# Performance work log

Hardware: AMD Instinct MI355X
Metric: run time of the kernel (lower is better)

The kernel has to match this reference:

```python
import jax, jax.numpy as jnp
import numpy as np

N = 50000       # nodes
E = 1_600_000   # edges (avg degree 32)
NFEAT = 256
NHID = 128
NCLASS = 128    # must equal NHID for the gated skip connection to type-check


def setup_inputs() -> dict:
    key = jax.random.key(0)
    ks = jax.random.split(key, 16)
    g = 0.02  # xavier gain used in the module
    inp = {
        "x": jax.random.normal(ks[0], (N, NFEAT), dtype=jnp.float32),
        "row": jax.random.randint(ks[1], (E,), 0, N, dtype=jnp.int32),
        "col": jax.random.randint(ks[2], (E,), 0, N, dtype=jnp.int32),
        # GatedSkipConnection params (shared across the three skip calls)
        "W_sc": jax.random.normal(ks[3], (NFEAT, NHID), dtype=jnp.float32) * 0.05,
        "W_ci": jax.random.normal(ks[4], (NHID, NHID), dtype=jnp.float32) * 0.05,
        "b_ci": jnp.zeros((NHID,), dtype=jnp.float32),
        "W_co": jax.random.normal(ks[5], (NHID, NHID), dtype=jnp.float32) * 0.05,
        "b_co": jnp.zeros((NHID,), dtype=jnp.float32),
        # GraphSAGE layer weights: [2*in, out], bias [1, out] (init to 0 per module)
        "W0": jax.random.normal(ks[6], (2 * NFEAT, NHID), dtype=jnp.float32) * g,
        "b0": jnp.zeros((1, NHID), dtype=jnp.float32),
        "W1": jax.random.normal(ks[7], (2 * NHID, NHID), dtype=jnp.float32) * g,
        "b1": jnp.zeros((1, NHID), dtype=jnp.float32),
        "W2": jax.random.normal(ks[8], (2 * NHID, NCLASS), dtype=jnp.float32) * g,
        "b2": jnp.zeros((1, NCLASS), dtype=jnp.float32),
        # fc0: Linear(nhid, nclass)
        "Wf": jax.random.normal(ks[9], (NHID, NCLASS), dtype=jnp.float32) * 0.05,
        "bf": jnp.zeros((NCLASS,), dtype=jnp.float32),
    }
    return inp


def _sage(x, row, col, inv_deg, W, b):
    # adj @ x : sum source features x[col] into destination rows `row`
    agg = jax.ops.segment_sum(x[col], row, num_segments=N)  # [N, d]
    agg = agg * inv_deg[:, None]                            # degree normalization
    support = jnp.concatenate([x, agg], axis=1)             # [N, 2d]
    return support @ W + b


def _gsc(in_x, out_x, W_sc, W_ci, b_ci, W_co, b_co):
    in_x = in_x @ W_sc if in_x.shape[1] != out_x.shape[1] else in_x
    z = jax.nn.sigmoid(in_x @ W_ci + b_ci + out_x @ W_co + b_co)
    return z * out_x + (1.0 - z) * in_x


def reference(x, row, col, W_sc, W_ci, b_ci, W_co, b_co,
              W0, b0, W1, b1, W2, b2, Wf, bf):
    deg = jax.ops.segment_sum(jnp.ones((E,), x.dtype), row, num_segments=N)
    inv_deg = 1.0 / jnp.maximum(deg, 1.0)  # guard isolated nodes

    residual = x
    o1 = _sage(x, row, col, inv_deg, W0, b0)
    o3 = jax.nn.relu(_gsc(residual, o1, W_sc, W_ci, b_ci, W_co, b_co))
    o4 = _sage(o3, row, col, inv_deg, W1, b1)
    o6 = jax.nn.relu(_gsc(residual, o4, W_sc, W_ci, b_ci, W_co, b_co))
    o7 = _sage(o6, row, col, inv_deg, W2, b2)
    o8 = _gsc(residual, o7, W_sc, W_ci, b_ci, W_co, b_co)
    return o8 @ Wf + bf
```

## Files before the change

### kernel.cpp

```cpp
#include <hip/hip_runtime.h>
#include <hip/hip_bf16.h>
#include <hip/hip_fp16.h>
#include <math.h>

#define NN 50000
#define EE 1600000
#define NFEAT 256
#define NHID 128
#define RNG 12500
#define NPASS 4
#define CPAD 16

typedef _Float16 f16;
typedef _Float16 f16x8 __attribute__((ext_vector_type(8)));
typedef _Float16 f16x4 __attribute__((ext_vector_type(4)));
typedef float f32x4 __attribute__((ext_vector_type(4)));

struct WPtrs {
    const float* s[10];
    f16* d[10];
};

__global__ __launch_bounds__(256) void k_prep(const float* __restrict__ x,
                                              f16* __restrict__ xh, int n4,
                                              int* __restrict__ cnt, int nz4,
                                              WPtrs wp, int wtotal,
                                              int zb0, int wb0, int wblocks) {
    int b = blockIdx.x;
    if (b < zb0) {
        int i = b * 256 + threadIdx.x;
        if (i < n4) {
            float4 v = reinterpret_cast<const float4*>(x)[i];
            f16x4 h = {(f16)v.x, (f16)v.y, (f16)v.z, (f16)v.w};
            reinterpret_cast<f16x4*>(xh)[i] = h;
        }
    } else if (b < wb0) {
        int i = (b - zb0) * 256 + threadIdx.x;
        if (i < nz4) reinterpret_cast<int4*>(cnt)[i] = make_int4(0, 0, 0, 0);
    } else {
        for (int idx = (b - wb0) * 256 + threadIdx.x; idx < wtotal;
             idx += wblocks * 256) {
            int wsel, rem, K;
            if (idx < 3 * 32768) { wsel = idx >> 15; rem = idx & 32767; K = 256; }
            else { int t = idx - 3 * 32768; wsel = 3 + (t >> 14); rem = t & 16383; K = 128; }
            int k = rem >> 7, c = rem & 127;
            wp.d[wsel][c * K + k] = (f16)wp.s[wsel][rem];
        }
    }
}

__global__ void k_slot(const int* __restrict__ row, int* __restrict__ cnt,
                       int* __restrict__ epack, int e) {
    int i = blockIdx.x * 256 + threadIdx.x;
    if (i < e) {
        int r = row[i];
        int s = atomicAdd(&cnt[(size_t)r * CPAD], 1);
        epack[i] = (s << 16) | r;
    }
}

__global__ void k_scan1(const int* __restrict__ cnt, int* __restrict__ bsum, int n) {
    __shared__ int s[256];
    int t = threadIdx.x;
    int i = blockIdx.x * 256 + t;
    s[t] = (i < n) ? cnt[(size_t)i * CPAD] : 0;
    __syncthreads();
    for (int off = 128; off > 0; off >>= 1) {
        if (t < off) s[t] += s[t + off];
        __syncthreads();
    }
    if (t == 0) bsum[blockIdx.x] = s[0];
}

__global__ void k_scan3(const int* __restrict__ cnt, const int* __restrict__ bsum,
                        int* __restrict__ rp, float* __restrict__ invd,
                        int n, int nb) {
    __shared__ int buf[2][256];
    __shared__ int bpre[2][256];
    int t = threadIdx.x;

    bpre[0][t] = (t < nb) ? bsum[t] : 0;
    __syncthreads();
    int bs = 0;
    for (int off = 1; off < 256; off <<= 1) {
        int v = bpre[bs][t];
        if (t >= off) v += bpre[bs][t - off];
        bpre[bs ^ 1][t] = v;
        bs ^= 1;
        __syncthreads();
    }
    int base = (blockIdx.x == 0) ? 0 : bpre[bs][blockIdx.x - 1];

    int i = blockIdx.x * 256 + t;
    int v = (i < n) ? cnt[(size_t)i * CPAD] : 0;
    buf[0][t] = v;
    __syncthreads();
    int sel = 0;
    for (int off = 1; off < 256; off <<= 1) {
        int x = buf[sel][t];
        if (t >= off) x += buf[sel][t - off];
        buf[sel ^ 1][t] = x;
        sel ^= 1;
        __syncthreads();
    }
    int incl = buf[sel][t];
    int excl = incl - v;
    if (i < n) {
        rp[i] = base + excl;
        invd[i] = 1.0f / fmaxf((float)v, 1.0f);
        if (i == n - 1) rp[n] = base + incl;
    }
}

__global__ void k_fill(const int* __restrict__ epack, const int* __restrict__ col,
                       const int* __restrict__ rp, int* __restrict__ ci, int e) {
    int i = blockIdx.x * 256 + threadIdx.x;
    if (i >= e) return;
    int pk = epack[i];
    int r = pk & 0xFFFF;
    int lo = blockIdx.y * RNG;
    if (r >= lo && r < lo + RNG) ci[rp[r] + (pk >> 16)] = col[i];
}

__global__ __launch_bounds__(256) void k_agg2h(const f16* __restrict__ P,
                                               const int* __restrict__ rp,
                                               const int* __restrict__ ci,
                                               const float* __restrict__ invd,
                                               const f16* __restrict__ T,
                                               f16* __restrict__ OUT, int n) {
    int node = blockIdx.x * 16 + (threadIdx.x >> 4);
    if (node >= n) return;
    int lane = threadIdx.x & 15;
    int s = rp[node], e = rp[node + 1];
    float acc[8];
#pragma unroll
    for (int q = 0; q < 8; ++q) acc[q] = 0.0f;
    int j = s;
    for (; j + 8 <= e; j += 8) {
        f16x8 v[8];
#pragma unroll
        for (int u = 0; u < 8; ++u)
            v[u] = *reinterpret_cast<const f16x8*>(P + (size_t)ci[j + u] * 128 + lane * 8);
#pragma unroll
        for (int q = 0; q < 8; ++q)
            acc[q] += (((float)v[0][q] + (float)v[1][q]) + ((float)v[2][q] + (float)v[3][q])) +
                      (((float)v[4][q] + (float)v[5][q]) + ((float)v[6][q] + (float)v[7][q]));
    }
    for (; j < e; ++j) {
        f16x8 v0 = *reinterpret_cast<const f16x8*>(P + (size_t)ci[j] * 128 + lane * 8);
#pragma unroll
        for (int q = 0; q < 8; ++q) acc[q] += (float)v0[q];
    }
    float scl = invd[node];
    f16x8 tv = *reinterpret_cast<const f16x8*>(T + (size_t)node * 128 + lane * 8);
    f16x8 o;
#pragma unroll
    for (int q = 0; q < 8; ++q) o[q] = (f16)((float)tv[q] + scl * acc[q]);
    *reinterpret_cast<f16x8*>(OUT + (size_t)node * 128 + lane * 8) = o;
}

#define LDSSTR 40

__device__ __forceinline__ void stage_A(const f16* __restrict__ A, f16* sA,
                                        int row0, int K, int kb, int tid, int n) {
    int r = tid >> 2, ch = tid & 3;
    int gr = row0 + r;
    uint4 v = make_uint4(0, 0, 0, 0);
    if (gr < n) v = *reinterpret_cast<const uint4*>(A + (size_t)gr * K + kb + ch * 8);
    *reinterpret_cast<uint4*>(sA + r * LDSSTR + ch * 8) = v;
}

__device__ __forceinline__ void stage_B(const f16* __restrict__ Wt, f16* sB,
                                        int K, int kb, int tid) {
#pragma unroll
    for (int i = 0; i < 2; ++i) {
        int idx = tid + i * 256;
        int c = idx >> 2, ch = idx & 3;
        uint4 v = *reinterpret_cast<const uint4*>(Wt + (size_t)c * K + kb + ch * 8);
        *reinterpret_cast<uint4*>(sB + c * LDSSTR + ch * 8) = v;
    }
}

template <int K, int NW, bool F32OUT>
__global__ __launch_bounds__(256) void k_mgemm(const f16* __restrict__ A,
                                               const f16* __restrict__ Wt0,
                                               const f16* __restrict__ Wt1,
                                               const f16* __restrict__ Wt2,
                                               const float* __restrict__ bias0,
                                               void* __restrict__ C0,
                                               void* __restrict__ C1,
                                               void* __restrict__ C2, int n) {
    __shared__ f16 sA[64 * LDSSTR];
    __shared__ f16 sB[128 * LDSSTR];

    const f16* Wt = Wt0;
    const float* bias = bias0;
    void* C = C0;
    if (NW > 1 && blockIdx.y == 1) { Wt = Wt1; bias = nullptr; C = C1; }
    if (NW > 2 && blockIdx.y == 2) { Wt = Wt2; bias = nullptr; C = C2; }

    const int tid = threadIdx.x;
    const int row0 = blockIdx.x * 64;
    const int wid = tid >> 6, l = tid & 63;
    const int wr = wid >> 1, wc = wid & 1;
    const int lr = l & 15, lk = (l >> 4) * 8;

    f32x4 acc[2][4];
#pragma unroll
    for (int m = 0; m < 2; ++m)
#pragma unroll
        for (int q = 0; q < 4; ++q) acc[m][q] = (f32x4){0.f, 0.f, 0.f, 0.f};

    for (int kt = 0; kt < K / 32; ++kt) {
        stage_A(A, sA, row0, K, kt * 32, tid, n);
        stage_B(Wt, sB, K, kt * 32, tid);
        __syncthreads();
        f16x8 aF[2], bF[4];
#pragma unroll
        for (int m = 0; m < 2; ++m)
            aF[m] = *reinterpret_cast<f16x8*>(sA + (wr * 32 + m * 16 + lr) * LDSSTR + lk);
#pragma unroll
        for (int q = 0; q < 4; ++q)
            bF[q] = *reinterpret_cast<f16x8*>(sB + (wc * 64 + q * 16 + lr) * LDSSTR + lk);
#pragma unroll
        for (int m = 0; m < 2; ++m)
#pragma unroll
            for (int q = 0; q < 4; ++q)
                acc[m][q] = __builtin_amdgcn_mfma_f32_16x16x32_f16(aF[m], bF[q],
                                                                   acc[m][q], 0, 0, 0);
        __syncthreads();
    }

    const int lr4 = (l >> 4) * 4;
#pragma unroll
    for (int m = 0; m < 2; ++m)
#pragma unroll
        for (int q = 0; q < 4; ++q) {
            int c = wc * 64 + q * 16 + (l & 15);
            float b = bias ? bias[c] : 0.0f;
#pragma unroll
            for (int reg = 0; reg < 4; ++reg) {
                int r = row0 + wr * 32 + m * 16 + lr4 + reg;
                if (r >= n) continue;
                float v = acc[m][q][reg] + b;
                if (F32OUT) ((float*)C)[(size_t)r * 128 + c] = v;
                else        ((f16*)C)[(size_t)r * 128 + c] = (f16)v;
            }
        }
}

#define FSTR 136

template <int RELU, bool CLS>
__global__ __launch_bounds__(256) void k_fused(const f16* __restrict__ Asc,
                                               const f16* __restrict__ At0,
                                               const f16* __restrict__ Wci,
                                               const f16* __restrict__ Wco,
                                               const f16* __restrict__ WtT,
                                               const f16* __restrict__ WtP,
                                               const float* __restrict__ bci,
                                               const float* __restrict__ bco,
                                               const float* __restrict__ bias2,
                                               f16* __restrict__ To,
                                               f16* __restrict__ Po,
                                               float* __restrict__ Fo, int n) {
    __shared__ f16 lsc[64 * FSTR];
    __shared__ f16 lt0[64 * FSTR];
    __shared__ f16 lt1[64 * FSTR];

    const int tid = threadIdx.x;
    const int row0 = blockIdx.x * 64;
    const int wid = tid >> 6, l = tid & 63;
    const int wr = wid >> 1, wc = wid & 1;
    const int lr = l & 15, lk = (l >> 4) * 8;
    const int lr4 = (l >> 4) * 4;

#pragma unroll
    for (int i = 0; i < 4; ++i) {
        int idx = tid + i * 256;
        int r = idx >> 4, ch = idx & 15;
        int gr = row0 + r;
        uint4 vs = make_uint4(0, 0, 0, 0), vt = make_uint4(0, 0, 0, 0);
        if (gr < n) {
            vs = *reinterpret_cast<const uint4*>(Asc + (size_t)gr * 128 + ch * 8);
            vt = *reinterpret_cast<const uint4*>(At0 + (size_t)gr * 128 + ch * 8);
        }
        *reinterpret_cast<uint4*>(lsc + r * FSTR + ch * 8) = vs;
        *reinterpret_cast<uint4*>(lt0 + r * FSTR + ch * 8) = vt;
    }
    __syncthreads();

    f32x4 accG[2][4];
#pragma unroll
    for (int m = 0; m < 2; ++m)
#pragma unroll
        for (int q = 0; q < 4; ++q) accG[m][q] = (f32x4){0.f, 0.f, 0.f, 0.f};

#pragma unroll
    for (int kt = 0; kt < 4; ++kt) {
        f16x8 aS[2], aT[2], bC[4], bO[4];
#pragma unroll
        for (int m = 0; m < 2; ++m) {
            int rr = (wr * 32 + m * 16 + lr) * FSTR + kt * 32 + lk;
            aS[m] = *reinterpret_cast<const f16x8*>(lsc + rr);
            aT[m] = *reinterpret_cast<const f16x8*>(lt0 + rr);
        }
#pragma unroll
        for (int q = 0; q < 4; ++q) {
            int c = wc * 64 + q * 16 + lr;
            bC[q] = *reinterpret_cast<const f16x8*>(Wci + (size_t)c * 128 + kt * 32 + lk);
            bO[q] = *reinterpret_cast<const f16x8*>(Wco + (size_t)c * 128 + kt * 32 + lk);
        }
#pragma unroll
        for (int m = 0; m < 2; ++m)
#pragma unroll
            for (int q = 0; q < 4; ++q) {
                accG[m][q] = __builtin_amdgcn_mfma_f32_16x16x32_f16(aS[m], bC[q],
                                                                    accG[m][q], 0, 0, 0);
                accG[m][q] = __builtin_amdgcn_mfma_f32_16x16x32_f16(aT[m], bO[q],
                                                                    accG[m][q], 0, 0, 0);
            }
    }

#pragma unroll
    for (int m = 0; m < 2; ++m)
#pragma unroll
        for (int q = 0; q < 4; ++q) {
            int c = wc * 64 + q * 16 + (l & 15);
            float bb = bci[c] + bco[c];
#pragma unroll
            for (int reg = 0; reg < 4; ++reg) {
                int lrow = wr * 32 + m * 16 + lr4 + reg;
                float v = accG[m][q][reg] + bb;
                float z = 1.0f / (1.0f + __expf(-v));
                float o = (float)lt0[lrow * FSTR + c];
                float s = (float)lsc[lrow * FSTR + c];
                float t1v = z * o + (1.0f - z) * s;
                if (RELU) t1v = fmaxf(t1v, 0.0f);
                lt1[lrow * FSTR + c] = (f16)t1v;
            }
        }
    __syncthreads();

    f32x4 accT[2][4], accP[2][4];
#pragma unroll
    for (int m = 0; m < 2; ++m)
#pragma unroll
        for (int q = 0; q < 4; ++q) {
            accT[m][q] = (f32x4){0.f, 0.f, 0.f, 0.f};
            accP[m][q] = (f32x4){0.f, 0.f, 0.f, 0.f};
        }

#pragma unroll
    for (int kt = 0; kt < 4; ++kt) {
        f16x8 aF[2], bT[4], bP[4];
#pragma unroll
        for (int m = 0; m < 2; ++m)
            aF[m] = *reinterpret_cast<const f16x8*>(
                lt1 + (wr * 32 + m * 16 + lr) * FSTR + kt * 32 + lk);
#pragma unroll
        for (int q = 0; q < 4; ++q) {
            int c = wc * 64 + q * 16 + lr;
            bT[q] = *reinterpret_cast<const f16x8*>(WtT + (size_t)c * 128 + kt * 32 + lk);
            if (!CLS)
                bP[q] = *reinterpret_cast<const f16x8*>(WtP + (size_t)c * 128 + kt * 32 + lk);
        }
#pragma unroll
        for (int m = 0; m < 2; ++m)
#pragma unroll
            for (int q = 0; q < 4; ++q) {
                accT[m][q] = __builtin_amdgcn_mfma_f32_16x16x32_f16(aF[m], bT[q],
                                                                    accT[m][q], 0, 0, 0);
                if (!CLS)
                    accP[m][q] = __builtin_amdgcn_mfma_f32_16x16x32_f16(aF[m], bP[q],
                                                                        accP[m][q], 0, 0, 0);
            }
    }

#pragma unroll
    for (int m = 0; m < 2; ++m)
#pragma unroll
        for (int q = 0; q < 4; ++q) {
            int c = wc * 64 + q * 16 + (l & 15);
            float b = bias2[c];
#pragma unroll
            for (int reg = 0; reg < 4; ++reg) {
                int r = row0 + wr * 32 + m * 16 + lr4 + reg;
                if (r >= n) continue;
                if (CLS) {
                    Fo[(size_t)r * 128 + c] = accT[m][q][reg] + b;
                } else {
                    To[(size_t)r * 128 + c] = (f16)(accT[m][q][reg] + b);
                    Po[(size_t)r * 128 + c] = (f16)accP[m][q][reg];
                }
            }
        }
}

extern "C" void kernel_launch(void* const* d_in, const int* in_sizes, int n_in,
                              void* d_out, int out_size, void* d_ws, size_t ws_size,
                              hipStream_t stream) {
    const float* x    = (const float*)d_in[0];
    const int*   row  = (const int*)d_in[1];
    const int*   col  = (const int*)d_in[2];
    const float* W_sc = (const float*)d_in[3];
    const float* W_ci = (const float*)d_in[4];
    const float* b_ci = (const float*)d_in[5];
    const float* W_co = (const float*)d_in[6];
    const float* b_co = (const float*)d_in[7];
    const float* W0   = (const float*)d_in[8];
    const float* b0   = (const float*)d_in[9];
    const float* W1   = (const float*)d_in[10];
    const float* b1   = (const float*)d_in[11];
    const float* W2   = (const float*)d_in[12];
    const float* b2   = (const float*)d_in[13];
    const float* Wf   = (const float*)d_in[14];
    const float* bf   = (const float*)d_in[15];
    float* out = (float*)d_out;

    char* p = (char*)d_ws;
    auto alloc = [&](size_t bytes) {
        char* q = p;
        p += (bytes + 255) & ~(size_t)255;
        return q;
    };
    int*   cnt   = (int*)alloc((size_t)NN * CPAD * 4);
    int*   rp    = (int*)alloc((NN + 1) * 4);
    int*   bsum  = (int*)alloc(256 * 4);
    float* invd  = (float*)alloc(NN * 4);
    int*   ci    = (int*)alloc(EE * 4);
    int*   epack = (int*)alloc(EE * 4);
    f16*   x_h   = (f16*)alloc((size_t)NN * 256 * 2);
    f16*   sc_h  = (f16*)alloc((size_t)NN * 128 * 2);
    f16*   T_h   = (f16*)alloc((size_t)NN * 128 * 2);
    f16*   P_h   = (f16*)alloc((size_t)NN * 128 * 2);
    f16*   t0_h  = (f16*)alloc((size_t)NN * 128 * 2);
    f16* W0t_t = (f16*)alloc(256 * 128 * 2);
    f16* W0b_t = (f16*)alloc(256 * 128 * 2);
    f16* Wsc_t = (f16*)alloc(256 * 128 * 2);
    f16* W1t_t = (f16*)alloc(128 * 128 * 2);
    f16* W1b_t = (f16*)alloc(128 * 128 * 2);
    f16* W2t_t = (f16*)alloc(128 * 128 * 2);
    f16* W2b_t = (f16*)alloc(128 * 128 * 2);
    f16* Wci_t = (f16*)alloc(128 * 128 * 2);
    f16* Wco_t = (f16*)alloc(128 * 128 * 2);
    f16* Wf_t  = (f16*)alloc(128 * 128 * 2);

    const int NB_N  = (NN + 255) / 256;
    const int NB_E  = (EE + 255) / 256;
    const int GB    = (NN + 63) / 64;
    const int AGG_B = (NN + 15) / 16;

    const int N4   = NN * 256 / 4;
    const int NZ4  = NN * CPAD / 4;
    const int ZB0  = (N4 + 255) / 256;
    const int WB0  = ZB0 + (NZ4 + 255) / 256;
    const int WBLK = 84;
    const int WTOT = 3 * 32768 + 7 * 16384;
    WPtrs wp;
    wp.s[0] = W0;             wp.d[0] = W0t_t;
    wp.s[1] = W0 + 256 * 128; wp.d[1] = W0b_t;
    wp.s[2] = W_sc;           wp.d[2] = Wsc_t;
    wp.s[3] = W1;             wp.d[3] = W1t_t;
    wp.s[4] = W1 + 128 * 128; wp.d[4] = W1b_t;
    wp.s[5] = W2;             wp.d[5] = W2t_t;
    wp.s[6] = W2 + 128 * 128; wp.d[6] = W2b_t;
    wp.s[7] = W_ci;           wp.d[7] = Wci_t;
    wp.s[8] = W_co;           wp.d[8] = Wco_t;
    wp.s[9] = Wf;             wp.d[9] = Wf_t;
    k_prep<<<WB0 + WBLK, 256, 0, stream>>>(x, x_h, N4, cnt, NZ4, wp, WTOT,
                                           ZB0, WB0, WBLK);

    k_slot<<<NB_E, 256, 0, stream>>>(row, cnt, epack, EE);
    k_scan1<<<NB_N, 256, 0, stream>>>(cnt, bsum, NN);
    k_scan3<<<NB_N, 256, 0, stream>>>(cnt, bsum, rp, invd, NN, NB_N);
    k_fill<<<dim3(NB_E, NPASS), 256, 0, stream>>>(epack, col, rp, ci, EE);

    k_mgemm<256, 3, false><<<dim3(GB, 3), 256, 0, stream>>>(
        x_h, W0t_t, W0b_t, Wsc_t, b0, T_h, P_h, sc_h, NN);
    k_agg2h<<<AGG_B, 256, 0, stream>>>(P_h, rp, ci, invd, T_h, t0_h, NN);

    k_fused<1, false><<<GB, 256, 0, stream>>>(
        sc_h, t0_h, Wci_t, Wco_t, W1t_t, W1b_t, b_ci, b_co, b1,
        T_h, P_h, nullptr, NN);
    k_agg2h<<<AGG_B, 256, 0, stream>>>(P_h, rp, ci, invd, T_h, t0_h, NN);

    k_fused<1, false><<<GB, 256, 0, stream>>>(
        sc_h, t0_h, Wci_t, Wco_t, W2t_t, W2b_t, b_ci, b_co, b2,
        T_h, P_h, nullptr, NN);
    k_agg2h<<<AGG_B, 256, 0, stream>>>(P_h, rp, ci, invd, T_h, t0_h, NN);

    k_fused<0, true><<<GB, 256, 0, stream>>>(
        sc_h, t0_h, Wci_t, Wco_t, Wf_t, nullptr, b_ci, b_co, bf,
        nullptr, nullptr, out, NN);
}
```

Before: 544.7 us.

## Fuse edge slotting with first GEMM and shuffle-broadcast neighbor indices in aggregation

Merges the atomic edge-slot kernel and the first three-way GEMM into one launch, interleaving GEMM blocks among slot blocks so the memory-bound atomics overlap with MFMA work and one launch is removed. The aggregation kernel now loads 16 neighbor indices cooperatively per 16-lane group and broadcasts them with shuffles, issuing 16 gathers in flight instead of 8 with per-lane redundant index loads. The tail handles the remainder with clamped indices and predicated accumulation. This raises register pressure in the aggregation kernel and makes the fused kernel's register and LDS footprint apply to the slot blocks as well.

```diff
diff --git a/kernel.cpp b/kernel.cpp
--- a/kernel.cpp
+++ b/kernel.cpp
@@ -10,6 +10,9 @@
 #define RNG 12500
 #define NPASS 4
 #define CPAD 16
+#define GB 782
+#define NGEMM (GB * 3)
+#define NB_E 6250
 
 typedef _Float16 f16;
 typedef _Float16 f16x8 __attribute__((ext_vector_type(8)));
@@ -49,13 +52,118 @@
     }
 }
 
-__global__ void k_slot(const int* __restrict__ row, int* __restrict__ cnt,
-                       int* __restrict__ epack, int e) {
-    int i = blockIdx.x * 256 + threadIdx.x;
-    if (i < e) {
-        int r = row[i];
-        int s = atomicAdd(&cnt[(size_t)r * CPAD], 1);
-        epack[i] = (s << 16) | r;
+#define LDSSTR 40
+
+__device__ __forceinline__ void stage_A(const f16* __restrict__ A, f16* sA,
+                                        int row0, int K, int kb, int tid, int n) {
+    int r = tid >> 2, ch = tid & 3;
+    int gr = row0 + r;
+    uint4 v = make_uint4(0, 0, 0, 0);
+    if (gr < n) v = *reinterpret_cast<const uint4*>(A + (size_t)gr * K + kb + ch * 8);
+    *reinterpret_cast<uint4*>(sA + r * LDSSTR + ch * 8) = v;
+}
+
+__device__ __forceinline__ void stage_B(const f16* __restrict__ Wt, f16* sB,
+                                        int K, int kb, int tid) {
+#pragma unroll
+    for (int i = 0; i < 2; ++i) {
+        int idx = tid + i * 256;
+        int c = idx >> 2, ch = idx & 3;
+        uint4 v = *reinterpret_cast<const uint4*>(Wt + (size_t)c * K + kb + ch * 8);
+        *reinterpret_cast<uint4*>(sB + c * LDSSTR + ch * 8) = v;
+    }
+}
+
+__device__ void gemm0_body(int bx, int by, f16* sA, f16* sB,
+                           const f16* __restrict__ A,
+                           const f16* __restrict__ Wt0,
+                           const f16* __restrict__ Wt1,
+                           const f16* __restrict__ Wt2,
+                           const float* __restrict__ bias0,
+                           f16* __restrict__ C0, f16* __restrict__ C1,
+                           f16* __restrict__ C2, int n) {
+    constexpr int K = 256;
+    const f16* Wt = Wt0;
+    const float* bias = bias0;
+    f16* C = C0;
+    if (by == 1) { Wt = Wt1; bias = nullptr; C = C1; }
+    if (by == 2) { Wt = Wt2; bias = nullptr; C = C2; }
+
+    const int tid = threadIdx.x;
+    const int row0 = bx * 64;
+    const int wid = tid >> 6, l = tid & 63;
+    const int wr = wid >> 1, wc = wid & 1;
+    const int lr = l & 15, lk = (l >> 4) * 8;
+
+    f32x4 acc[2][4];
+#pragma unroll
+    for (int m = 0; m < 2; ++m)
+#pragma unroll
+        for (int q = 0; q < 4; ++q) acc[m][q] = (f32x4){0.f, 0.f, 0.f, 0.f};
+
+    for (int kt = 0; kt < K / 32; ++kt) {
+        stage_A(A, sA, row0, K, kt * 32, tid, n);
+        stage_B(Wt, sB, K, kt * 32, tid);
+        __syncthreads();
+        f16x8 aF[2], bF[4];
+#pragma unroll
+        for (int m = 0; m < 2; ++m)
+            aF[m] = *reinterpret_cast<f16x8*>(sA + (wr * 32 + m * 16 + lr) * LDSSTR + lk);
+#pragma unroll
+        for (int q = 0; q < 4; ++q)
+            bF[q] = *reinterpret_cast<f16x8*>(sB + (wc * 64 + q * 16 + lr) * LDSSTR + lk);
+#pragma unroll
+        for (int m = 0; m < 2; ++m)
+#pragma unroll
+            for (int q = 0; q < 4; ++q)
+                acc[m][q] = __builtin_amdgcn_mfma_f32_16x16x32_f16(aF[m], bF[q],
+                                                                   acc[m][q], 0, 0, 0);
+        __syncthreads();
+    }
+
+    const int lr4 = (l >> 4) * 4;
+#pragma unroll
+    for (int m = 0; m < 2; ++m)
+#pragma unroll
+        for (int q = 0; q < 4; ++q) {
+            int c = wc * 64 + q * 16 + (l & 15);
+            float b = bias ? bias[c] : 0.0f;
+#pragma unroll
+            for (int reg = 0; reg < 4; ++reg) {
+                int r = row0 + wr * 32 + m * 16 + lr4 + reg;
+                if (r >= n) continue;
+                C[(size_t)r * 128 + c] = (f16)(acc[m][q][reg] + b);
+            }
+        }
+}
+
+__global__ __launch_bounds__(256) void k_slotgemm(
+    const int* __restrict__ row, int* __restrict__ cnt,
+    int* __restrict__ epack, int e,
+    const f16* __restrict__ A,
+    const f16* __restrict__ Wt0, const f16* __restrict__ Wt1,
+    const f16* __restrict__ Wt2, const float* __restrict__ bias0,
+    f16* __restrict__ C0, f16* __restrict__ C1, f16* __restrict__ C2, int n) {
+    __shared__ f16 sA[64 * LDSSTR];
+    __shared__ f16 sB[128 * LDSSTR];
+
+    int p = blockIdx.x / 11, k = blockIdx.x % 11;
+    bool isG = (k == 2) || (k == 6) || (k == 9);
+    if (isG) {
+        int idx = (k == 2) ? 0 : ((k == 6) ? 1 : 2);
+        int g = p * 3 + idx;
+        if (g >= NGEMM) return;
+        gemm0_body(g % GB, g / GB, sA, sB, A, Wt0, Wt1, Wt2, bias0, C0, C1, C2, n);
+    } else {
+        int rank = k - (k > 2) - (k > 6) - (k > 9);
+        int s = p * 8 + rank;
+        if (s >= NB_E) return;
+        int i = s * 256 + threadIdx.x;
+        if (i < e) {
+            int r = row[i];
+            int sl = atomicAdd(&cnt[(size_t)r * CPAD], 1);
+            epack[i] = (sl << 16) | r;
+        }
     }
 }
 
@@ -135,118 +243,43 @@
     float acc[8];
 #pragma unroll
     for (int q = 0; q < 8; ++q) acc[q] = 0.0f;
+
     int j = s;
-    for (; j + 8 <= e; j += 8) {
-        f16x8 v[8];
-#pragma unroll
-        for (int u = 0; u < 8; ++u)
-            v[u] = *reinterpret_cast<const f16x8*>(P + (size_t)ci[j + u] * 128 + lane * 8);
-#pragma unroll
-        for (int q = 0; q < 8; ++q)
-            acc[q] += (((float)v[0][q] + (float)v[1][q]) + ((float)v[2][q] + (float)v[3][q])) +
-                      (((float)v[4][q] + (float)v[5][q]) + ((float)v[6][q] + (float)v[7][q]));
-    }
-    for (; j < e; ++j) {
-        f16x8 v0 = *reinterpret_cast<const f16x8*>(P + (size_t)ci[j] * 128 + lane * 8);
-#pragma unroll
-        for (int q = 0; q < 8; ++q) acc[q] += (float)v0[q];
-    }
+    for (; j + 16 <= e; j += 16) {
+        int civ = ci[j + lane];
+        f16x8 v[16];
+#pragma unroll
+        for (int u = 0; u < 16; ++u) {
+            int nb = __shfl(civ, u, 16);
+            v[u] = *reinterpret_cast<const f16x8*>(P + (size_t)nb * 128 + lane * 8);
+        }
+#pragma unroll
+        for (int u = 0; u < 16; ++u)
+#pragma unroll
+            for (int q = 0; q < 8; ++q) acc[q] += (float)v[u][q];
+    }
+    int rem = e - j;
+    if (rem > 0) {
+        int civ = ci[j + (lane < rem ? lane : rem - 1)];
+        f16x8 v[16];
+#pragma unroll
+        for (int u = 0; u < 16; ++u) {
+            int nb = __shfl(civ, u, 16);
+            v[u] = *reinterpret_cast<const f16x8*>(P + (size_t)nb * 128 + lane * 8);
+        }
+#pragma unroll
+        for (int u = 0; u < 16; ++u)
+            if (u < rem)
+#pragma unroll
+                for (int q = 0; q < 8; ++q) acc[q] += (float)v[u][q];
+    }
+
     float scl = invd[node];
     f16x8 tv = *reinterpret_cast<const f16x8*>(T + (size_t)node * 128 + lane * 8);
     f16x8 o;
 #pragma unroll
     for (int q = 0; q < 8; ++q) o[q] = (f16)((float)tv[q] + scl * acc[q]);
     *reinterpret_cast<f16x8*>(OUT + (size_t)node * 128 + lane * 8) = o;
-}
-
-#define LDSSTR 40
-
-__device__ __forceinline__ void stage_A(const f16* __restrict__ A, f16* sA,
-                                        int row0, int K, int kb, int tid, int n) {
-    int r = tid >> 2, ch = tid & 3;
-    int gr = row0 + r;
-    uint4 v = make_uint4(0, 0, 0, 0);
-    if (gr < n) v = *reinterpret_cast<const uint4*>(A + (size_t)gr * K + kb + ch * 8);
-    *reinterpret_cast<uint4*>(sA + r * LDSSTR + ch * 8) = v;
-}
-
-__device__ __forceinline__ void stage_B(const f16* __restrict__ Wt, f16* sB,
-                                        int K, int kb, int tid) {
-#pragma unroll
-    for (int i = 0; i < 2; ++i) {
-        int idx = tid + i * 256;
-        int c = idx >> 2, ch = idx & 3;
-        uint4 v = *reinterpret_cast<const uint4*>(Wt + (size_t)c * K + kb + ch * 8);
-        *reinterpret_cast<uint4*>(sB + c * LDSSTR + ch * 8) = v;
-    }
-}
-
-template <int K, int NW, bool F32OUT>
-__global__ __launch_bounds__(256) void k_mgemm(const f16* __restrict__ A,
-                                               const f16* __restrict__ Wt0,
-                                               const f16* __restrict__ Wt1,
-                                               const f16* __restrict__ Wt2,
-                                               const float* __restrict__ bias0,
-                                               void* __restrict__ C0,
-                                               void* __restrict__ C1,
-                                               void* __restrict__ C2, int n) {
-    __shared__ f16 sA[64 * LDSSTR];
-    __shared__ f16 sB[128 * LDSSTR];
-
-    const f16* Wt = Wt0;
-    const float* bias = bias0;
-    void* C = C0;
-    if (NW > 1 && blockIdx.y == 1) { Wt = Wt1; bias = nullptr; C = C1; }
-    if (NW > 2 && blockIdx.y == 2) { Wt = Wt2; bias = nullptr; C = C2; }
-
-    const int tid = threadIdx.x;
-    const int row0 = blockIdx.x * 64;
-    const int wid = tid >> 6, l = tid & 63;
-    const int wr = wid >> 1, wc = wid & 1;
-    const int lr = l & 15, lk = (l >> 4) * 8;
-
-    f32x4 acc[2][4];
-#pragma unroll
-    for (int m = 0; m < 2; ++m)
-#pragma unroll
-        for (int q = 0; q < 4; ++q) acc[m][q] = (f32x4){0.f, 0.f, 0.f, 0.f};
-
-    for (int kt = 0; kt < K / 32; ++kt) {
-        stage_A(A, sA, row0, K, kt * 32, tid, n);
-        stage_B(Wt, sB, K, kt * 32, tid);
-        __syncthreads();
-        f16x8 aF[2], bF[4];
-#pragma unroll
-        for (int m = 0; m < 2; ++m)
-            aF[m] = *reinterpret_cast<f16x8*>(sA + (wr * 32 + m * 16 + lr) * LDSSTR + lk);
-#pragma unroll
-        for (int q = 0; q < 4; ++q)
-            bF[q] = *reinterpret_cast<f16x8*>(sB + (wc * 64 + q * 16 + lr) * LDSSTR + lk);
-#pragma unroll
-        for (int m = 0; m < 2; ++m)
-#pragma unroll
-            for (int q = 0; q < 4; ++q)
-                acc[m][q] = __builtin_amdgcn_mfma_f32_16x16x32_f16(aF[m], bF[q],
-                                                                   acc[m][q], 0, 0, 0);
-        __syncthreads();
-    }
-
-    const int lr4 = (l >> 4) * 4;
-#pragma unroll
-    for (int m = 0; m < 2; ++m)
-#pragma unroll
-        for (int q = 0; q < 4; ++q) {
-            int c = wc * 64 + q * 16 + (l & 15);
-            float b = bias ? bias[c] : 0.0f;
-#pragma unroll
-            for (int reg = 0; reg < 4; ++reg) {
-                int r = row0 + wr * 32 + m * 16 + lr4 + reg;
-                if (r >= n) continue;
-                float v = acc[m][q][reg] + b;
-                if (F32OUT) ((float*)C)[(size_t)r * 128 + c] = v;
-                else        ((f16*)C)[(size_t)r * 128 + c] = (f16)v;
-            }
-        }
 }
 
 #define FSTR 136
@@ -447,9 +480,8 @@
     f16* Wf_t  = (f16*)alloc(128 * 128 * 2);
 
     const int NB_N  = (NN + 255) / 256;
-    const int NB_E  = (EE + 255) / 256;
-    const int GB    = (NN + 63) / 64;
     const int AGG_B = (NN + 15) / 16;
+    const int MGRID = GB * 11;
 
     const int N4   = NN * 256 / 4;
     const int NZ4  = NN * CPAD / 4;
@@ -471,13 +503,14 @@
     k_prep<<<WB0 + WBLK, 256, 0, stream>>>(x, x_h, N4, cnt, NZ4, wp, WTOT,
                                            ZB0, WB0, WBLK);
 
-    k_slot<<<NB_E, 256, 0, stream>>>(row, cnt, epack, EE);
+    k_slotgemm<<<MGRID, 256, 0, stream>>>(row, cnt, epack, EE,
+                                          x_h, W0t_t, W0b_t, Wsc_t, b0,
+                                          T_h, P_h, sc_h, NN);
+
     k_scan1<<<NB_N, 256, 0, stream>>>(cnt, bsum, NN);
     k_scan3<<<NB_N, 256, 0, stream>>>(cnt, bsum, rp, invd, NN, NB_N);
     k_fill<<<dim3(NB_E, NPASS), 256, 0, stream>>>(epack, col, rp, ci, EE);
 
-    k_mgemm<256, 3, false><<<dim3(GB, 3), 256, 0, stream>>>(
-        x_h, W0t_t, W0b_t, Wsc_t, b0, T_h, P_h, sc_h, NN);
     k_agg2h<<<AGG_B, 256, 0, stream>>>(P_h, rp, ci, invd, T_h, t0_h, NN);
 
     k_fused<1, false><<<GB, 256, 0, stream>>>(
```

Result: faster. 512.3 us (-5.9%).
